# Optimization experiments

Measured on AMD Instinct MI355X. Metric: run time of the kernel, lower is better.

Reference implementation:

```python
import jax, jax.numpy as jnp
import numpy as np

D_MODEL = 512
N_HEADS = 8
HEAD_DIM = D_MODEL // N_HEADS
D_FF = 2048
EPS = 1e-5


def layer_norm(x, gamma, beta):
    mu = jnp.mean(x, axis=-1, keepdims=True)
    var = jnp.mean((x - mu) ** 2, axis=-1, keepdims=True)
    return (x - mu) * jax.lax.rsqrt(var + EPS) * gamma + beta


def setup_inputs() -> dict:
    key = jax.random.key(0)
    ks = jax.random.split(key, 17)
    B, S = 2, 2048
    s_in = 1.0 / np.sqrt(D_MODEL)
    s_ff = 1.0 / np.sqrt(D_FF)
    return {
        "x": jax.random.normal(ks[0], (B, S, D_MODEL), jnp.float32),
        "Wq": jax.random.normal(ks[1], (D_MODEL, D_MODEL), jnp.float32) * s_in,
        "bq": jnp.zeros((D_MODEL,), jnp.float32),
        "Wk": jax.random.normal(ks[2], (D_MODEL, D_MODEL), jnp.float32) * s_in,
        "bk": jnp.zeros((D_MODEL,), jnp.float32),
        "Wv": jax.random.normal(ks[3], (D_MODEL, D_MODEL), jnp.float32) * s_in,
        "bv": jnp.zeros((D_MODEL,), jnp.float32),
        "Wo": jax.random.normal(ks[4], (D_MODEL, D_MODEL), jnp.float32) * s_in,
        "bo": jnp.zeros((D_MODEL,), jnp.float32),
        "W1": jax.random.normal(ks[5], (D_MODEL, D_FF), jnp.float32) * s_in,
        "b1": jnp.zeros((D_FF,), jnp.float32),
        "W2": jax.random.normal(ks[6], (D_FF, D_MODEL), jnp.float32) * s_ff,
        "b2": jnp.zeros((D_MODEL,), jnp.float32),
        "g1": jnp.ones((D_MODEL,), jnp.float32),
        "be1": jnp.zeros((D_MODEL,), jnp.float32),
        "g2": jnp.ones((D_MODEL,), jnp.float32),
        "be2": jnp.zeros((D_MODEL,), jnp.float32),
    }


def reference(x, Wq, bq, Wk, bk, Wv, bv, Wo, bo, W1, b1, W2, b2, g1, be1, g2, be2):
    B, S, _ = x.shape
    # projections + split heads -> [B, H, S, Dh]
    def heads(t):
        return t.reshape(B, S, N_HEADS, HEAD_DIM).transpose(0, 2, 1, 3)
    q = heads(x @ Wq + bq)
    k = heads(x @ Wk + bk)
    v = heads(x @ Wv + bv)
    # explicit scaled dot-product attention (full [B,H,S,S] scores as in source)
    scores = jnp.einsum('bhqd,bhkd->bhqk', q, k) / np.sqrt(HEAD_DIM).astype(np.float32)
    attn = jax.nn.softmax(scores, axis=-1)
    ctx = jnp.einsum('bhqk,bhkd->bhqd', attn, v)
    ctx = ctx.transpose(0, 2, 1, 3).reshape(B, S, D_MODEL)
    attn_out = ctx @ Wo + bo
    # post-norm residual 1
    h = layer_norm(x + attn_out, g1, be1)
    # FFN
    ff = jax.nn.relu(h @ W1 + b1) @ W2 + b2
    # post-norm residual 2
    return layer_norm(h + ff, g2, be2)
```

## Files before the change

kernel.cpp:

```cpp
#include <hip/hip_runtime.h>
#include <cmath>

#define D_MODEL 512
#define N_HEADS 8
#define HEAD_DIM 64
#define D_FF 2048
#define SEQ 2048
#define BATCH 2
#define MROWS (BATCH * SEQ)

typedef __attribute__((ext_vector_type(8))) short short8;
typedef __attribute__((ext_vector_type(4))) float float4v;
typedef unsigned short ushort_t;

static __device__ __forceinline__ ushort_t f2bf(float f) {
    union { float f; unsigned u; } v; v.f = f;
    unsigned r = (v.u + 0x7FFFu + ((v.u >> 16) & 1u)) >> 16;
    return (ushort_t)r;
}
static __device__ __forceinline__ ushort_t f2bf_trunc(float f) {
    union { float f; unsigned u; } v; v.f = f;
    return (ushort_t)(v.u >> 16);
}

static __device__ __forceinline__ void gload16(const void* g, void* l) {
    __builtin_amdgcn_global_load_lds(
        (__attribute__((address_space(1))) void*)(unsigned long long)g,
        (__attribute__((address_space(3))) void*)(unsigned)(unsigned long long)l,
        16, 0, 0);
}

__global__ __launch_bounds__(256) void prep_k(
    const float* __restrict__ x,
    const float* __restrict__ Wq, const float* __restrict__ Wk,
    const float* __restrict__ Wv, const float* __restrict__ Wo,
    const float* __restrict__ W1, const float* __restrict__ W2,
    ushort_t* __restrict__ xb,
    ushort_t* __restrict__ WqkvT, ushort_t* __restrict__ WoT,
    ushort_t* __restrict__ W1T, ushort_t* __restrict__ W2T)
{
    int tile = blockIdx.x;
    if (tile >= 3072) {
        int i = (tile - 3072) * 256 + threadIdx.x;
        float4 f = ((const float4*)x)[i];
        ushort4 o;
        o.x = f2bf(f.x); o.y = f2bf(f.y); o.z = f2bf(f.z); o.w = f2bf(f.w);
        ((ushort4*)xb)[i] = o;
        return;
    }
    const float* src; ushort_t* dst; int Kd, Nd, tloc;
    if (tile < 1024) {
        int wsel = tile >> 8; tloc = tile & 255; Kd = 512; Nd = 512;
        if (wsel == 0)      { src = Wq; dst = WqkvT; }
        else if (wsel == 1) { src = Wk; dst = WqkvT + (size_t)512 * 512; }
        else if (wsel == 2) { src = Wv; dst = WqkvT + (size_t)1024 * 512; }
        else                { src = Wo; dst = WoT; }
    } else if (tile < 2048) { tloc = tile - 1024; Kd = 512;  Nd = 2048; src = W1; dst = W1T; }
    else                    { tloc = tile - 2048; Kd = 2048; Nd = 512;  src = W2; dst = W2T; }
    int tn = Nd >> 5;
    int k0 = (tloc / tn) << 5, n0 = (tloc % tn) << 5;
    __shared__ float tl[32][33];
    int c = threadIdx.x & 31, r = threadIdx.x >> 5;
    #pragma unroll
    for (int i = 0; i < 4; ++i)
        tl[r + i * 8][c] = src[(size_t)(k0 + r + i * 8) * Nd + n0 + c];
    __syncthreads();
    #pragma unroll
    for (int i = 0; i < 4; ++i)
        dst[(size_t)(n0 + r + i * 8) * Kd + k0 + c] = f2bf(tl[c][r + i * 8]);
}

template <int BN, int NT, int MODE>
__global__ __launch_bounds__(256) void gemm_std_k(
    const ushort_t* __restrict__ A, const ushort_t* __restrict__ BT,
    const float* __restrict__ bias, void* __restrict__ Cv,
    int N, int K, int Klen, size_t zstride)
{
    __shared__ ushort_t As[128 * 32];
    __shared__ ushort_t Bs[BN * 32];

    const int t = threadIdx.x;
    const int w = t >> 6, lane = t & 63, l16 = lane & 15, quad = lane >> 4;
    const int m0 = blockIdx.y * 128;
    const int n0 = blockIdx.x * BN;
    const int kbase = blockIdx.z * Klen;
    const int mbase = (w >> 1) * 64;
    const int nbase = (w & 1) * (NT * 16);
    const int srow = lane >> 2;
    const int schk = (lane & 3) * 8;

    float4v acc[4][NT];
    #pragma unroll
    for (int mt = 0; mt < 4; ++mt)
        #pragma unroll
        for (int nt = 0; nt < NT; ++nt)
            acc[mt][nt] = (float4v){0.f, 0.f, 0.f, 0.f};

    for (int ks = kbase; ks < kbase + Klen; ks += 32) {
        __syncthreads();
        #pragma unroll
        for (int g = 0; g < 2; ++g)
            gload16(A + (size_t)(m0 + g * 64 + w * 16 + srow) * K + ks + schk,
                    &As[g * 2048 + w * 512]);
        #pragma unroll
        for (int g = 0; g < BN / 64; ++g)
            gload16(BT + (size_t)(n0 + g * 64 + w * 16 + srow) * K + ks + schk,
                    &Bs[g * 2048 + w * 512]);
        __syncthreads();

        short8 af[4], bf8[NT];
        #pragma unroll
        for (int mt = 0; mt < 4; ++mt)
            af[mt] = *(const short8*)&As[(mbase + mt * 16 + l16) * 32 + quad * 8];
        #pragma unroll
        for (int nt = 0; nt < NT; ++nt)
            bf8[nt] = *(const short8*)&Bs[(nbase + nt * 16 + l16) * 32 + quad * 8];
        #pragma unroll
        for (int mt = 0; mt < 4; ++mt)
            #pragma unroll
            for (int nt = 0; nt < NT; ++nt)
                acc[mt][nt] = __builtin_amdgcn_mfma_f32_16x16x32_bf16(
                    af[mt], bf8[nt], acc[mt][nt], 0, 0, 0);
    }

    float* Cf = (float*)Cv + blockIdx.z * zstride;
    #pragma unroll
    for (int mt = 0; mt < 4; ++mt) {
        #pragma unroll
        for (int nt = 0; nt < NT; ++nt) {
            int gcol = n0 + nbase + nt * 16 + l16;
            float b = (MODE == 2) ? 0.f : bias[gcol];
            #pragma unroll
            for (int r = 0; r < 4; ++r) {
                int grow = m0 + mbase + mt * 16 + quad * 4 + r;
                float v = acc[mt][nt][r] + b;
                if (MODE == 1) v = fmaxf(v, 0.f);
                if (MODE == 1) ((ushort_t*)Cv)[(size_t)grow * N + gcol] = f2bf(v);
                else           Cf[(size_t)grow * N + gcol] = v;
            }
        }
    }
}

__global__ __launch_bounds__(256) void gemm_qkv_k(
    const ushort_t* __restrict__ A, const ushort_t* __restrict__ BT,
    const float* __restrict__ bq, const float* __restrict__ bk,
    const float* __restrict__ bv,
    ushort_t* __restrict__ Qb, ushort_t* __restrict__ Kb,
    ushort_t* __restrict__ VTb)
{
    __shared__ ushort_t As[128 * 32];
    __shared__ ushort_t Bs[128 * 32];

    const int t = threadIdx.x;
    const int w = t >> 6, lane = t & 63, l16 = lane & 15, quad = lane >> 4;
    const int m0 = blockIdx.y * 128;
    const int n0 = blockIdx.x * 128;
    const int mbase = (w >> 1) * 64;
    const int nbase = (w & 1) * 64;
    const int srow = lane >> 2;
    const int schk = (lane & 3) * 8;
    const int K = 512;

    float4v acc[4][4];
    #pragma unroll
    for (int mt = 0; mt < 4; ++mt)
        #pragma unroll
        for (int nt = 0; nt < 4; ++nt)
            acc[mt][nt] = (float4v){0.f, 0.f, 0.f, 0.f};

    for (int ks = 0; ks < 512; ks += 32) {
        __syncthreads();
        #pragma unroll
        for (int g = 0; g < 2; ++g)
            gload16(A + (size_t)(m0 + g * 64 + w * 16 + srow) * K + ks + schk,
                    &As[g * 2048 + w * 512]);
        #pragma unroll
        for (int g = 0; g < 2; ++g)
            gload16(BT + (size_t)(n0 + g * 64 + w * 16 + srow) * K + ks + schk,
                    &Bs[g * 2048 + w * 512]);
        __syncthreads();

        short8 af[4], bf8[4];
        #pragma unroll
        for (int mt = 0; mt < 4; ++mt)
            af[mt] = *(const short8*)&As[(mbase + mt * 16 + l16) * 32 + quad * 8];
        #pragma unroll
        for (int nt = 0; nt < 4; ++nt)
            bf8[nt] = *(const short8*)&Bs[(nbase + nt * 16 + l16) * 32 + quad * 8];
        #pragma unroll
        for (int mt = 0; mt < 4; ++mt)
            #pragma unroll
            for (int nt = 0; nt < 4; ++nt)
                acc[mt][nt] = __builtin_amdgcn_mfma_f32_16x16x32_bf16(
                    af[mt], bf8[nt], acc[mt][nt], 0, 0, 0);
    }

    const int tsel = n0 >> 9;
    const float* bias = (tsel == 0) ? bq : (tsel == 1) ? bk : bv;
    const float scl = (tsel == 0) ? 0.18033688f : 1.0f;
    ushort_t* dst = (tsel == 0) ? Qb : Kb;

    #pragma unroll
    for (int mt = 0; mt < 4; ++mt) {
        #pragma unroll
        for (int nt = 0; nt < 4; ++nt) {
            int gcol = n0 + nbase + nt * 16 + l16;
            int lcol = gcol - (tsel << 9);
            int h = lcol >> 6, dh = lcol & 63;
            float b = bias[lcol];
            #pragma unroll
            for (int r = 0; r < 4; ++r) {
                int grow = m0 + mbase + mt * 16 + quad * 4 + r;
                int bb = grow >> 11, s = grow & 2047;
                float v = (acc[mt][nt][r] + b) * scl;
                if (tsel < 2)
                    dst[(((size_t)(bb * N_HEADS + h)) * SEQ + s) * HEAD_DIM + dh] = f2bf(v);
                else
                    VTb[(((size_t)(bb * N_HEADS + h)) * HEAD_DIM + dh) * SEQ + s] = f2bf(v);
            }
        }
    }
}

__global__ __launch_bounds__(256) void attn_mfma_k(
    const ushort_t* __restrict__ Qg, const ushort_t* __restrict__ Kg,
    const ushort_t* __restrict__ VTg,
    float* __restrict__ Opart, float* __restrict__ Lpart)
{
    __shared__ __align__(16) ushort_t Kbuf[2][64 * 64];
    __shared__ __align__(16) ushort_t Vbuf[2][64 * 64];
    __shared__ __align__(16) ushort_t Ps[4][16 * 64];

    const int bh = blockIdx.x;
    const int q0 = blockIdx.y * 64;
    const int ks = blockIdx.z;
    const int t = threadIdx.x;
    const int w = t >> 6;
    const int lane = t & 63;
    const int l16 = lane & 15;
    const int quad = lane >> 4;
    const int qbase = q0 + w * 16;
    const float M2 = 14.4269504f;

    const int r0 = t >> 3;
    const int r1 = r0 + 32;
    const int g0 = (t & 7) ^ (r0 & 7);
    const int g1 = (t & 7) ^ (r1 & 7);
    const size_t kgrow = (size_t)bh * SEQ;
    const size_t vgrow = (size_t)bh * HEAD_DIM;

#define ATTN_STAGE(b, kb)                                                       \
    {                                                                           \
        gload16(Kg + (kgrow + (kb) + r0) * HEAD_DIM + g0 * 8, &Kbuf[b][w * 512]);          \
        gload16(Kg + (kgrow + (kb) + r1) * HEAD_DIM + g1 * 8, &Kbuf[b][2048 + w * 512]);   \
        gload16(VTg + (vgrow + r0) * SEQ + (kb) + g0 * 8, &Vbuf[b][w * 512]);              \
        gload16(VTg + (vgrow + r1) * SEQ + (kb) + g1 * 8, &Vbuf[b][2048 + w * 512]);       \
    }

    short8 aq[2];
    {
        const ushort_t* qp = Qg + ((size_t)bh * SEQ + qbase + l16) * HEAD_DIM + quad * 8;
        aq[0] = *(const short8*)(qp);
        aq[1] = *(const short8*)(qp + 32);
    }

    float4v o[4] = {};
    float l_acc[4] = {0.f, 0.f, 0.f, 0.f};

    ATTN_STAGE(0, ks * 1024)

    for (int kt = 0; kt < 16; ++kt) {
        const int cur = kt & 1;
        if (kt < 15) {
            ATTN_STAGE(cur ^ 1, ks * 1024 + (kt + 1) * 64)
            asm volatile("s_waitcnt vmcnt(4)" ::: "memory");
        } else {
            asm volatile("s_waitcnt vmcnt(0)" ::: "memory");
        }
        asm volatile("s_barrier" ::: "memory");

        const ushort_t* Kc = Kbuf[cur];
        const ushort_t* Vc = Vbuf[cur];

        float4v s[4];
        #pragma unroll
        for (int nt = 0; nt < 4; ++nt) s[nt] = (float4v){0.f, 0.f, 0.f, 0.f};
        #pragma unroll
        for (int c = 0; c < 2; ++c) {
            const int poff = (((c * 4 + quad) ^ (l16 & 7)) << 3);
            #pragma unroll
            for (int nt = 0; nt < 4; ++nt) {
                short8 bk8 = *(const short8*)&Kc[(nt * 16 + l16) * 64 + poff];
                s[nt] = __builtin_amdgcn_mfma_f32_16x16x32_bf16(aq[c], bk8, s[nt], 0, 0, 0);
            }
        }

        #pragma unroll
        for (int nt = 0; nt < 4; ++nt) {
            #pragma unroll
            for (int r = 0; r < 4; ++r) {
                float p = exp2f(s[nt][r] - M2);
                s[nt][r] = p;
                l_acc[r] += p;
            }
        }

        #pragma unroll
        for (int nt = 0; nt < 4; ++nt)
            #pragma unroll
            for (int r = 0; r < 4; ++r) {
                int row = quad * 4 + r;
                int key = nt * 16 + l16;
                Ps[w][row * 64 + (((key >> 3) ^ (row & 7)) << 3) + (key & 7)] =
                    f2bf_trunc(s[nt][r]);
            }
        asm volatile("s_waitcnt lgkmcnt(0)" ::: "memory");

        #pragma unroll
        for (int c = 0; c < 2; ++c) {
            short8 ap = *(const short8*)&Ps[w][l16 * 64 + ((((c << 2) + quad) ^ (l16 & 7)) << 3)];
            const int poff = (((c * 4 + quad) ^ (l16 & 7)) << 3);
            #pragma unroll
            for (int dt = 0; dt < 4; ++dt) {
                short8 bv8 = *(const short8*)&Vc[(dt * 16 + l16) * 64 + poff];
                o[dt] = __builtin_amdgcn_mfma_f32_16x16x32_bf16(ap, bv8, o[dt], 0, 0, 0);
            }
        }

        asm volatile("s_barrier" ::: "memory");
    }
#undef ATTN_STAGE

    const size_t pbase = ((size_t)(ks * 16 + bh)) * SEQ;
    #pragma unroll
    for (int r = 0; r < 4; ++r) {
        float L = l_acc[r];
        #pragma unroll
        for (int msk = 1; msk < 16; msk <<= 1) L += __shfl_xor(L, msk);
        int qrow = qbase + quad * 4 + r;
        if (l16 == 0) Lpart[pbase + qrow] = L;
        #pragma unroll
        for (int dt = 0; dt < 4; ++dt)
            Opart[(pbase + qrow) * HEAD_DIM + dt * 16 + l16] = o[dt][r];
    }
}

__global__ __launch_bounds__(256) void attn_comb_k(
    const float* __restrict__ Op, const float* __restrict__ Lp,
    ushort_t* __restrict__ ctx)
{
    int g = blockIdx.x * 256 + threadIdx.x;
    int d4 = g & 15;
    int q  = (g >> 4) & 2047;
    int bh = g >> 15;
    float ax = 0.f, ay = 0.f, az = 0.f, aw = 0.f, L = 0.f;
    #pragma unroll
    for (int ks = 0; ks < 2; ++ks) {
        size_t row = ((size_t)(ks * 16 + bh) * SEQ + q) * HEAD_DIM;
        float4 a = ((const float4*)(Op + row))[d4];
        ax += a.x; ay += a.y; az += a.z; aw += a.w;
        L += Lp[ks * 16 * SEQ + bh * SEQ + q];
    }
    float inv = 1.0f / L;
    ushort4 o4;
    o4.x = f2bf(ax * inv);
    o4.y = f2bf(ay * inv);
    o4.z = f2bf(az * inv);
    o4.w = f2bf(aw * inv);
    int bb = bh >> 3, hh = bh & 7;
    *(ushort4*)&ctx[((size_t)(bb * SEQ + q)) * D_MODEL + hh * HEAD_DIM + d4 * 4] = o4;
}

template <int WRITE_BF>
__global__ __launch_bounds__(256) void add_ln_k(
    const float* __restrict__ X, const float* __restrict__ P0,
    const float* __restrict__ P1, const float* __restrict__ bias,
    const float* __restrict__ gam, const float* __restrict__ bet,
    float* __restrict__ O, ushort_t* __restrict__ Ob)
{
    const int row = blockIdx.x;
    const int t = threadIdx.x;
    const size_t ro = (size_t)row * D_MODEL;

    float v0 = X[ro + t]       + P0[ro + t]       + P1[ro + t]       + bias[t];
    float v1 = X[ro + t + 256] + P0[ro + t + 256] + P1[ro + t + 256] + bias[t + 256];
    float s = v0 + v1;
    float ss = v0 * v0 + v1 * v1;
    #pragma unroll
    for (int off = 32; off > 0; off >>= 1) {
        s  += __shfl_down(s, off);
        ss += __shfl_down(ss, off);
    }
    __shared__ float sb[4], ssb[4];
    if ((t & 63) == 0) { sb[t >> 6] = s; ssb[t >> 6] = ss; }
    __syncthreads();
    float S  = sb[0] + sb[1] + sb[2] + sb[3];
    float SS = ssb[0] + ssb[1] + ssb[2] + ssb[3];
    float mu  = S * (1.0f / D_MODEL);
    float var = SS * (1.0f / D_MODEL) - mu * mu;
    float inv = rsqrtf(var + 1e-5f);
    float o0 = (v0 - mu) * inv * gam[t] + bet[t];
    float o1 = (v1 - mu) * inv * gam[t + 256] + bet[t + 256];
    O[ro + t]       = o0;
    O[ro + t + 256] = o1;
    if (WRITE_BF) {
        Ob[ro + t]       = f2bf(o0);
        Ob[ro + t + 256] = f2bf(o1);
    }
}

extern "C" void kernel_launch(void* const* d_in, const int* in_sizes, int n_in,
                              void* d_out, int out_size, void* d_ws, size_t ws_size,
                              hipStream_t stream)
{
    const float* x   = (const float*)d_in[0];
    const float* Wq  = (const float*)d_in[1];
    const float* bq  = (const float*)d_in[2];
    const float* Wk  = (const float*)d_in[3];
    const float* bk  = (const float*)d_in[4];
    const float* Wv  = (const float*)d_in[5];
    const float* bv  = (const float*)d_in[6];
    const float* Wo  = (const float*)d_in[7];
    const float* bo  = (const float*)d_in[8];
    const float* W1  = (const float*)d_in[9];
    const float* b1  = (const float*)d_in[10];
    const float* W2  = (const float*)d_in[11];
    const float* b2  = (const float*)d_in[12];
    const float* g1  = (const float*)d_in[13];
    const float* be1 = (const float*)d_in[14];
    const float* g2  = (const float*)d_in[15];
    const float* be2 = (const float*)d_in[16];
    float* out = (float*)d_out;
    float* ws  = (float*)d_ws;

    ushort_t* WoT   = (ushort_t*)(ws);
    ushort_t* W1T   = (ushort_t*)(ws + 131072);
    ushort_t* W2T   = (ushort_t*)(ws + 655360);
    ushort_t* WqkvT = (ushort_t*)(ws + 1179648);
    ushort_t* xb    = (ushort_t*)(ws + 1572864);
    ushort_t* Qb    = (ushort_t*)(ws + 2621440);
    ushort_t* Kb    = (ushort_t*)(ws + 3670016);
    ushort_t* VTb   = (ushort_t*)(ws + 4718592);
    ushort_t* Ctx   = (ushort_t*)(ws + 5767168);
    float*    Lpart = ws + 6815744;
    float*    Hh    = ws + 6881280;
    float*    P0    = ws + 8978432;
    float*    P1    = ws + 11075584;
    float*    Opart = ws + 8978432;
    ushort_t* FF1   = (ushort_t*)(ws + 1572864);
    ushort_t* Hhb   = (ushort_t*)(ws + 5767168);

    prep_k<<<5120, 256, 0, stream>>>(x, Wq, Wk, Wv, Wo, W1, W2, xb, WqkvT, WoT, W1T, W2T);

    gemm_qkv_k<<<dim3(12, 32), 256, 0, stream>>>(xb, WqkvT, bq, bk, bv, Qb, Kb, VTb);

    attn_mfma_k<<<dim3(16, 32, 2), 256, 0, stream>>>(Qb, Kb, VTb, Opart, Lpart);
    attn_comb_k<<<2048, 256, 0, stream>>>(Opart, Lpart, Ctx);

    gemm_std_k<64, 2, 2><<<dim3(8, 32, 2), 256, 0, stream>>>(
        Ctx, WoT, nullptr, P0, 512, 512, 256, (size_t)MROWS * D_MODEL);

    add_ln_k<1><<<4096, 256, 0, stream>>>(x, P0, P1, bo, g1, be1, Hh, Hhb);

    gemm_std_k<128, 4, 1><<<dim3(16, 32), 256, 0, stream>>>(
        Hhb, W1T, b1, FF1, 2048, 512, 512, 0);

    gemm_std_k<64, 2, 2><<<dim3(8, 32, 2), 256, 0, stream>>>(
        FF1, W2T, nullptr, P0, 512, 2048, 1024, (size_t)MROWS * D_MODEL);

    add_ln_k<0><<<4096, 256, 0, stream>>>(Hh, P0, P1, b2, g2, be2, out, (ushort_t*)nullptr);
}
```

Measured before the change: 229.1 us.

## Fuse the whole layer into one persistent cooperative kernel with grid syncs

```diff
diff --git a/kernel.cpp b/kernel.cpp
--- a/kernel.cpp
+++ b/kernel.cpp
@@ -1,5 +1,8 @@
 #include <hip/hip_runtime.h>
+#include <hip/hip_cooperative_groups.h>
 #include <cmath>
+
+namespace cg = cooperative_groups;
 
 #define D_MODEL 512
 #define N_HEADS 8
@@ -29,6 +32,437 @@
         (__attribute__((address_space(3))) void*)(unsigned)(unsigned long long)l,
         16, 0, 0);
 }
+
+
+template <int MODE>
+__device__ void gemm64_stage(
+    const ushort_t* __restrict__ A, const ushort_t* __restrict__ BT,
+    const float* __restrict__ bias, void* __restrict__ Cv,
+    int N, int K, int m0, int n0, int kbase, int Klen, size_t zoff,
+    ushort_t* __restrict__ sm)
+{
+    ushort_t* As = sm;
+    ushort_t* Bs = sm + 4096;
+
+    const int t = threadIdx.x;
+    const int w = t >> 6, lane = t & 63, l16 = lane & 15, quad = lane >> 4;
+    const int mbase = (w >> 1) * 64;
+    const int nbase = (w & 1) * 32;
+    const int srow = lane >> 2;
+    const int schk = (lane & 3) * 8;
+
+    float4v acc[4][2];
+    #pragma unroll
+    for (int mt = 0; mt < 4; ++mt)
+        #pragma unroll
+        for (int nt = 0; nt < 2; ++nt)
+            acc[mt][nt] = (float4v){0.f, 0.f, 0.f, 0.f};
+
+    for (int ks = kbase; ks < kbase + Klen; ks += 32) {
+        __syncthreads();
+        #pragma unroll
+        for (int g = 0; g < 2; ++g)
+            gload16(A + (size_t)(m0 + g * 64 + w * 16 + srow) * K + ks + schk,
+                    &As[g * 2048 + w * 512]);
+        gload16(BT + (size_t)(n0 + w * 16 + srow) * K + ks + schk, &Bs[w * 512]);
+        __syncthreads();
+
+        short8 af[4], bf8[2];
+        #pragma unroll
+        for (int mt = 0; mt < 4; ++mt)
+            af[mt] = *(const short8*)&As[(mbase + mt * 16 + l16) * 32 + quad * 8];
+        #pragma unroll
+        for (int nt = 0; nt < 2; ++nt)
+            bf8[nt] = *(const short8*)&Bs[(nbase + nt * 16 + l16) * 32 + quad * 8];
+        #pragma unroll
+        for (int mt = 0; mt < 4; ++mt)
+            #pragma unroll
+            for (int nt = 0; nt < 2; ++nt)
+                acc[mt][nt] = __builtin_amdgcn_mfma_f32_16x16x32_bf16(
+                    af[mt], bf8[nt], acc[mt][nt], 0, 0, 0);
+    }
+
+    #pragma unroll
+    for (int mt = 0; mt < 4; ++mt) {
+        #pragma unroll
+        for (int nt = 0; nt < 2; ++nt) {
+            int gcol = n0 + nbase + nt * 16 + l16;
+            float b = (MODE == 2) ? 0.f : bias[gcol];
+            #pragma unroll
+            for (int r = 0; r < 4; ++r) {
+                int grow = m0 + mbase + mt * 16 + quad * 4 + r;
+                float v = acc[mt][nt][r] + b;
+                if (MODE == 1) {
+                    v = fmaxf(v, 0.f);
+                    ((ushort_t*)Cv)[(size_t)grow * N + gcol] = f2bf(v);
+                } else {
+                    ((float*)Cv + zoff)[(size_t)grow * N + gcol] = v;
+                }
+            }
+        }
+    }
+}
+
+__device__ void qkv64_stage(
+    const ushort_t* __restrict__ A, const ushort_t* __restrict__ BT,
+    const float* __restrict__ bq, const float* __restrict__ bk,
+    const float* __restrict__ bv,
+    ushort_t* __restrict__ Qb, ushort_t* __restrict__ Kb,
+    ushort_t* __restrict__ VTb,
+    int m0, int n0, ushort_t* __restrict__ sm)
+{
+    ushort_t* As = sm;
+    ushort_t* Bs = sm + 4096;
+
+    const int t = threadIdx.x;
+    const int w = t >> 6, lane = t & 63, l16 = lane & 15, quad = lane >> 4;
+    const int mbase = (w >> 1) * 64;
+    const int nbase = (w & 1) * 32;
+    const int srow = lane >> 2;
+    const int schk = (lane & 3) * 8;
+    const int K = 512;
+
+    float4v acc[4][2];
+    #pragma unroll
+    for (int mt = 0; mt < 4; ++mt)
+        #pragma unroll
+        for (int nt = 0; nt < 2; ++nt)
+            acc[mt][nt] = (float4v){0.f, 0.f, 0.f, 0.f};
+
+    for (int ks = 0; ks < 512; ks += 32) {
+        __syncthreads();
+        #pragma unroll
+        for (int g = 0; g < 2; ++g)
+            gload16(A + (size_t)(m0 + g * 64 + w * 16 + srow) * K + ks + schk,
+                    &As[g * 2048 + w * 512]);
+        gload16(BT + (size_t)(n0 + w * 16 + srow) * K + ks + schk, &Bs[w * 512]);
+        __syncthreads();
+
+        short8 af[4], bf8[2];
+        #pragma unroll
+        for (int mt = 0; mt < 4; ++mt)
+            af[mt] = *(const short8*)&As[(mbase + mt * 16 + l16) * 32 + quad * 8];
+        #pragma unroll
+        for (int nt = 0; nt < 2; ++nt)
+            bf8[nt] = *(const short8*)&Bs[(nbase + nt * 16 + l16) * 32 + quad * 8];
+        #pragma unroll
+        for (int mt = 0; mt < 4; ++mt)
+            #pragma unroll
+            for (int nt = 0; nt < 2; ++nt)
+                acc[mt][nt] = __builtin_amdgcn_mfma_f32_16x16x32_bf16(
+                    af[mt], bf8[nt], acc[mt][nt], 0, 0, 0);
+    }
+
+    const int tsel = n0 >> 9;
+    const float* bias = (tsel == 0) ? bq : (tsel == 1) ? bk : bv;
+    const float scl = (tsel == 0) ? 0.18033688f : 1.0f;
+    ushort_t* dst = (tsel == 0) ? Qb : Kb;
+
+    #pragma unroll
+    for (int mt = 0; mt < 4; ++mt) {
+        #pragma unroll
+        for (int nt = 0; nt < 2; ++nt) {
+            int gcol = n0 + nbase + nt * 16 + l16;
+            int lcol = gcol - (tsel << 9);
+            int h = lcol >> 6, dh = lcol & 63;
+            float b = bias[lcol];
+            #pragma unroll
+            for (int r = 0; r < 4; ++r) {
+                int grow = m0 + mbase + mt * 16 + quad * 4 + r;
+                int bb = grow >> 11, s = grow & 2047;
+                float v = (acc[mt][nt][r] + b) * scl;
+                if (tsel < 2)
+                    dst[(((size_t)(bb * N_HEADS + h)) * SEQ + s) * HEAD_DIM + dh] = f2bf(v);
+                else
+                    VTb[(((size_t)(bb * N_HEADS + h)) * HEAD_DIM + dh) * SEQ + s] = f2bf(v);
+            }
+        }
+    }
+}
+
+__device__ void attn_stage(
+    const ushort_t* __restrict__ Qg, const ushort_t* __restrict__ Kg,
+    const ushort_t* __restrict__ VTg,
+    float* __restrict__ Opart, float* __restrict__ Lpart,
+    int bh, int q0, int ks, ushort_t* __restrict__ sm)
+{
+    ushort_t* Kbp[2] = { sm, sm + 4096 };
+    ushort_t* Vbp[2] = { sm + 8192, sm + 12288 };
+    const int t = threadIdx.x;
+    const int w = t >> 6;
+    ushort_t* Psw = sm + 16384 + w * 1024;
+
+    const int lane = t & 63;
+    const int l16 = lane & 15;
+    const int quad = lane >> 4;
+    const int qbase = q0 + w * 16;
+    const float M2 = 14.4269504f;
+
+    const int r0 = t >> 3;
+    const int r1 = r0 + 32;
+    const int g0 = (t & 7) ^ (r0 & 7);
+    const int g1 = (t & 7) ^ (r1 & 7);
+    const size_t kgrow = (size_t)bh * SEQ;
+    const size_t vgrow = (size_t)bh * HEAD_DIM;
+
+#define ATTN_ST(b, kb)                                                                     \
+    {                                                                                      \
+        gload16(Kg + (kgrow + (kb) + r0) * HEAD_DIM + g0 * 8, Kbp[b] + w * 512);           \
+        gload16(Kg + (kgrow + (kb) + r1) * HEAD_DIM + g1 * 8, Kbp[b] + 2048 + w * 512);    \
+        gload16(VTg + (vgrow + r0) * SEQ + (kb) + g0 * 8, Vbp[b] + w * 512);               \
+        gload16(VTg + (vgrow + r1) * SEQ + (kb) + g1 * 8, Vbp[b] + 2048 + w * 512);        \
+    }
+
+    short8 aq[2];
+    {
+        const ushort_t* qp = Qg + ((size_t)bh * SEQ + qbase + l16) * HEAD_DIM + quad * 8;
+        aq[0] = *(const short8*)(qp);
+        aq[1] = *(const short8*)(qp + 32);
+    }
+
+    float4v o[4] = {};
+    float l_acc[4] = {0.f, 0.f, 0.f, 0.f};
+
+    ATTN_ST(0, ks * 1024)
+
+    for (int kt = 0; kt < 16; ++kt) {
+        const int cur = kt & 1;
+        if (kt < 15) {
+            ATTN_ST(cur ^ 1, ks * 1024 + (kt + 1) * 64)
+            asm volatile("s_waitcnt vmcnt(4)" ::: "memory");
+        } else {
+            asm volatile("s_waitcnt vmcnt(0)" ::: "memory");
+        }
+        asm volatile("s_barrier" ::: "memory");
+
+        const ushort_t* Kc = Kbp[cur];
+        const ushort_t* Vc = Vbp[cur];
+
+        float4v s[4];
+        #pragma unroll
+        for (int nt = 0; nt < 4; ++nt) s[nt] = (float4v){0.f, 0.f, 0.f, 0.f};
+        #pragma unroll
+        for (int c = 0; c < 2; ++c) {
+            const int poff = (((c * 4 + quad) ^ (l16 & 7)) << 3);
+            #pragma unroll
+            for (int nt = 0; nt < 4; ++nt) {
+                short8 bk8 = *(const short8*)&Kc[(nt * 16 + l16) * 64 + poff];
+                s[nt] = __builtin_amdgcn_mfma_f32_16x16x32_bf16(aq[c], bk8, s[nt], 0, 0, 0);
+            }
+        }
+
+        #pragma unroll
+        for (int nt = 0; nt < 4; ++nt) {
+            #pragma unroll
+            for (int r = 0; r < 4; ++r) {
+                float p = exp2f(s[nt][r] - M2);
+                s[nt][r] = p;
+                l_acc[r] += p;
+            }
+        }
+
+        #pragma unroll
+        for (int nt = 0; nt < 4; ++nt)
+            #pragma unroll
+            for (int r = 0; r < 4; ++r) {
+                int row = quad * 4 + r;
+                int key = nt * 16 + l16;
+                Psw[row * 64 + (((key >> 3) ^ (row & 7)) << 3) + (key & 7)] =
+                    f2bf_trunc(s[nt][r]);
+            }
+        asm volatile("s_waitcnt lgkmcnt(0)" ::: "memory");
+
+        #pragma unroll
+        for (int c = 0; c < 2; ++c) {
+            short8 ap = *(const short8*)&Psw[l16 * 64 + ((((c << 2) + quad) ^ (l16 & 7)) << 3)];
+            const int poff = (((c * 4 + quad) ^ (l16 & 7)) << 3);
+            #pragma unroll
+            for (int dt = 0; dt < 4; ++dt) {
+                short8 bv8 = *(const short8*)&Vc[(dt * 16 + l16) * 64 + poff];
+                o[dt] = __builtin_amdgcn_mfma_f32_16x16x32_bf16(ap, bv8, o[dt], 0, 0, 0);
+            }
+        }
+
+        asm volatile("s_barrier" ::: "memory");
+    }
+#undef ATTN_ST
+
+    const size_t pbase = ((size_t)(ks * 16 + bh)) * SEQ;
+    #pragma unroll
+    for (int r = 0; r < 4; ++r) {
+        float L = l_acc[r];
+        #pragma unroll
+        for (int msk = 1; msk < 16; msk <<= 1) L += __shfl_xor(L, msk);
+        int qrow = qbase + quad * 4 + r;
+        if (l16 == 0) Lpart[pbase + qrow] = L;
+        #pragma unroll
+        for (int dt = 0; dt < 4; ++dt)
+            Opart[(pbase + qrow) * HEAD_DIM + dt * 16 + l16] = o[dt][r];
+    }
+}
+
+template <int WRITE_BF>
+__device__ void ln_stage(
+    const float* __restrict__ X, const float* __restrict__ P0,
+    const float* __restrict__ P1, const float* __restrict__ bias,
+    const float* __restrict__ gam, const float* __restrict__ bet,
+    float* __restrict__ O, ushort_t* __restrict__ Ob, ushort_t* __restrict__ sm)
+{
+    float* sb = (float*)sm;
+    float* ssb = sb + 4;
+    const int t = threadIdx.x;
+    for (int row = blockIdx.x; row < MROWS; row += gridDim.x) {
+        const size_t ro = (size_t)row * D_MODEL;
+        float v0 = X[ro + t]       + P0[ro + t]       + P1[ro + t]       + bias[t];
+        float v1 = X[ro + t + 256] + P0[ro + t + 256] + P1[ro + t + 256] + bias[t + 256];
+        float s = v0 + v1;
+        float ss = v0 * v0 + v1 * v1;
+        #pragma unroll
+        for (int off = 32; off > 0; off >>= 1) {
+            s  += __shfl_down(s, off);
+            ss += __shfl_down(ss, off);
+        }
+        if ((t & 63) == 0) { sb[t >> 6] = s; ssb[t >> 6] = ss; }
+        __syncthreads();
+        float S  = sb[0] + sb[1] + sb[2] + sb[3];
+        float SS = ssb[0] + ssb[1] + ssb[2] + ssb[3];
+        float mu  = S * (1.0f / D_MODEL);
+        float var = SS * (1.0f / D_MODEL) - mu * mu;
+        float inv = rsqrtf(var + 1e-5f);
+        float o0 = (v0 - mu) * inv * gam[t] + bet[t];
+        float o1 = (v1 - mu) * inv * gam[t + 256] + bet[t + 256];
+        O[ro + t]       = o0;
+        O[ro + t + 256] = o1;
+        if (WRITE_BF) {
+            Ob[ro + t]       = f2bf(o0);
+            Ob[ro + t + 256] = f2bf(o1);
+        }
+        __syncthreads();
+    }
+}
+
+__global__ __launch_bounds__(256, 4) void mega_k(
+    const float* x,
+    const float* Wq, const float* bq, const float* Wk, const float* bk,
+    const float* Wv, const float* bv, const float* Wo, const float* bo,
+    const float* W1, const float* b1, const float* W2, const float* b2,
+    const float* g1, const float* be1, const float* g2, const float* be2,
+    float* out, float* ws)
+{
+    cg::grid_group grid = cg::this_grid();
+    __shared__ __align__(16) ushort_t sm[20480];
+
+    ushort_t* WoT   = (ushort_t*)(ws);
+    ushort_t* W1T   = (ushort_t*)(ws + 131072);
+    ushort_t* W2T   = (ushort_t*)(ws + 655360);
+    ushort_t* WqkvT = (ushort_t*)(ws + 1179648);
+    ushort_t* xb    = (ushort_t*)(ws + 1572864);
+    ushort_t* Qb    = (ushort_t*)(ws + 2621440);
+    ushort_t* Kb    = (ushort_t*)(ws + 3670016);
+    ushort_t* VTb   = (ushort_t*)(ws + 4718592);
+    ushort_t* Ctx   = (ushort_t*)(ws + 5767168);
+    float*    Lpart = ws + 6815744;
+    float*    Hh    = ws + 6881280;
+    float*    P0    = ws + 8978432;
+    float*    P1    = ws + 11075584;
+    float*    Opart = ws + 8978432;
+    ushort_t* FF1   = (ushort_t*)(ws + 1572864);
+    ushort_t* Hhb   = (ushort_t*)(ws + 5767168);
+
+    const int bid = blockIdx.x;
+    const int G = gridDim.x;
+    const int t = threadIdx.x;
+
+    for (int tile = bid; tile < 5120; tile += G) {
+        if (tile >= 3072) {
+            int i = (tile - 3072) * 256 + t;
+            float4 f = ((const float4*)x)[i];
+            ushort4 o;
+            o.x = f2bf(f.x); o.y = f2bf(f.y); o.z = f2bf(f.z); o.w = f2bf(f.w);
+            ((ushort4*)xb)[i] = o;
+        } else {
+            const float* src; ushort_t* dst; int Kd, Nd, tloc;
+            if (tile < 1024) {
+                int wsel = tile >> 8; tloc = tile & 255; Kd = 512; Nd = 512;
+                if (wsel == 0)      { src = Wq; dst = WqkvT; }
+                else if (wsel == 1) { src = Wk; dst = WqkvT + (size_t)512 * 512; }
+                else if (wsel == 2) { src = Wv; dst = WqkvT + (size_t)1024 * 512; }
+                else                { src = Wo; dst = WoT; }
+            } else if (tile < 2048) { tloc = tile - 1024; Kd = 512;  Nd = 2048; src = W1; dst = W1T; }
+            else                    { tloc = tile - 2048; Kd = 2048; Nd = 512;  src = W2; dst = W2T; }
+            int tn = Nd >> 5;
+            int k0 = (tloc / tn) << 5, n0 = (tloc % tn) << 5;
+            float* tl = (float*)sm;
+            int c = t & 31, r = t >> 5;
+            #pragma unroll
+            for (int i = 0; i < 4; ++i)
+                tl[(r + i * 8) * 33 + c] = src[(size_t)(k0 + r + i * 8) * Nd + n0 + c];
+            __syncthreads();
+            #pragma unroll
+            for (int i = 0; i < 4; ++i)
+                dst[(size_t)(n0 + r + i * 8) * Kd + k0 + c] = f2bf(tl[c * 33 + r + i * 8]);
+            __syncthreads();
+        }
+    }
+    grid.sync();
+
+    for (int u = bid; u < 768; u += G)
+        qkv64_stage(xb, WqkvT, bq, bk, bv, Qb, Kb, VTb, (u / 24) * 128, (u % 24) * 64, sm);
+    grid.sync();
+
+    for (int u = bid; u < 1024; u += G)
+        attn_stage(Qb, Kb, VTb, Opart, Lpart, u & 15, ((u >> 4) & 31) * 64, u >> 9, sm);
+    grid.sync();
+
+    for (int u = bid; u < 2048; u += G) {
+        int gidx = u * 256 + t;
+        int d4 = gidx & 15;
+        int q  = (gidx >> 4) & 2047;
+        int bh = gidx >> 15;
+        float ax = 0.f, ay = 0.f, az = 0.f, aw = 0.f, L = 0.f;
+        #pragma unroll
+        for (int ks = 0; ks < 2; ++ks) {
+            size_t row = ((size_t)(ks * 16 + bh) * SEQ + q) * HEAD_DIM;
+            float4 a = ((const float4*)(Opart + row))[d4];
+            ax += a.x; ay += a.y; az += a.z; aw += a.w;
+            L += Lpart[ks * 16 * SEQ + bh * SEQ + q];
+        }
+        float inv = 1.0f / L;
+        ushort4 o4;
+        o4.x = f2bf(ax * inv);
+        o4.y = f2bf(ay * inv);
+        o4.z = f2bf(az * inv);
+        o4.w = f2bf(aw * inv);
+        int bb = bh >> 3, hh = bh & 7;
+        *(ushort4*)&Ctx[((size_t)(bb * SEQ + q)) * D_MODEL + hh * HEAD_DIM + d4 * 4] = o4;
+    }
+    grid.sync();
+
+    for (int u = bid; u < 512; u += G) {
+        int n0 = (u & 7) * 64, m0 = ((u >> 3) & 31) * 128, z = u >> 8;
+        gemm64_stage<2>(Ctx, WoT, nullptr, P0, 512, 512, m0, n0, z * 256, 256,
+                        (size_t)z * 2097152, sm);
+    }
+    grid.sync();
+
+    ln_stage<1>(x, P0, P1, bo, g1, be1, Hh, Hhb, sm);
+    grid.sync();
+
+    for (int u = bid; u < 1024; u += G)
+        gemm64_stage<1>(Hhb, W1T, b1, FF1, 2048, 512, (u >> 5) * 128, (u & 31) * 64,
+                        0, 512, 0, sm);
+    grid.sync();
+
+    for (int u = bid; u < 512; u += G) {
+        int n0 = (u & 7) * 64, m0 = ((u >> 3) & 31) * 128, z = u >> 8;
+        gemm64_stage<2>(FF1, W2T, nullptr, P0, 512, 2048, m0, n0, z * 1024, 1024,
+                        (size_t)z * 2097152, sm);
+    }
+    grid.sync();
+
+    ln_stage<0>(Hh, P0, P1, b2, g2, be2, out, (ushort_t*)nullptr, sm);
+}
+
 
 __global__ __launch_bounds__(256) void prep_k(
     const float* __restrict__ x,
@@ -228,122 +662,9 @@
     const ushort_t* __restrict__ VTg,
     float* __restrict__ Opart, float* __restrict__ Lpart)
 {
-    __shared__ __align__(16) ushort_t Kbuf[2][64 * 64];
-    __shared__ __align__(16) ushort_t Vbuf[2][64 * 64];
-    __shared__ __align__(16) ushort_t Ps[4][16 * 64];
-
-    const int bh = blockIdx.x;
-    const int q0 = blockIdx.y * 64;
-    const int ks = blockIdx.z;
-    const int t = threadIdx.x;
-    const int w = t >> 6;
-    const int lane = t & 63;
-    const int l16 = lane & 15;
-    const int quad = lane >> 4;
-    const int qbase = q0 + w * 16;
-    const float M2 = 14.4269504f;
-
-    const int r0 = t >> 3;
-    const int r1 = r0 + 32;
-    const int g0 = (t & 7) ^ (r0 & 7);
-    const int g1 = (t & 7) ^ (r1 & 7);
-    const size_t kgrow = (size_t)bh * SEQ;
-    const size_t vgrow = (size_t)bh * HEAD_DIM;
-
-#define ATTN_STAGE(b, kb)                                                       \
-    {                                                                           \
-        gload16(Kg + (kgrow + (kb) + r0) * HEAD_DIM + g0 * 8, &Kbuf[b][w * 512]);          \
-        gload16(Kg + (kgrow + (kb) + r1) * HEAD_DIM + g1 * 8, &Kbuf[b][2048 + w * 512]);   \
-        gload16(VTg + (vgrow + r0) * SEQ + (kb) + g0 * 8, &Vbuf[b][w * 512]);              \
-        gload16(VTg + (vgrow + r1) * SEQ + (kb) + g1 * 8, &Vbuf[b][2048 + w * 512]);       \
-    }
-
-    short8 aq[2];
-    {
-        const ushort_t* qp = Qg + ((size_t)bh * SEQ + qbase + l16) * HEAD_DIM + quad * 8;
-        aq[0] = *(const short8*)(qp);
-        aq[1] = *(const short8*)(qp + 32);
-    }
-
-    float4v o[4] = {};
-    float l_acc[4] = {0.f, 0.f, 0.f, 0.f};
-
-    ATTN_STAGE(0, ks * 1024)
-
-    for (int kt = 0; kt < 16; ++kt) {
-        const int cur = kt & 1;
-        if (kt < 15) {
-            ATTN_STAGE(cur ^ 1, ks * 1024 + (kt + 1) * 64)
-            asm volatile("s_waitcnt vmcnt(4)" ::: "memory");
-        } else {
-            asm volatile("s_waitcnt vmcnt(0)" ::: "memory");
-        }
-        asm volatile("s_barrier" ::: "memory");
-
-        const ushort_t* Kc = Kbuf[cur];
-        const ushort_t* Vc = Vbuf[cur];
-
-        float4v s[4];
-        #pragma unroll
-        for (int nt = 0; nt < 4; ++nt) s[nt] = (float4v){0.f, 0.f, 0.f, 0.f};
-        #pragma unroll
-        for (int c = 0; c < 2; ++c) {
-            const int poff = (((c * 4 + quad) ^ (l16 & 7)) << 3);
-            #pragma unroll
-            for (int nt = 0; nt < 4; ++nt) {
-                short8 bk8 = *(const short8*)&Kc[(nt * 16 + l16) * 64 + poff];
-                s[nt] = __builtin_amdgcn_mfma_f32_16x16x32_bf16(aq[c], bk8, s[nt], 0, 0, 0);
-            }
-        }
-
-        #pragma unroll
-        for (int nt = 0; nt < 4; ++nt) {
-            #pragma unroll
-            for (int r = 0; r < 4; ++r) {
-                float p = exp2f(s[nt][r] - M2);
-                s[nt][r] = p;
-                l_acc[r] += p;
-            }
-        }
-
-        #pragma unroll
-        for (int nt = 0; nt < 4; ++nt)
-            #pragma unroll
-            for (int r = 0; r < 4; ++r) {
-                int row = quad * 4 + r;
-                int key = nt * 16 + l16;
-                Ps[w][row * 64 + (((key >> 3) ^ (row & 7)) << 3) + (key & 7)] =
-                    f2bf_trunc(s[nt][r]);
-            }
-        asm volatile("s_waitcnt lgkmcnt(0)" ::: "memory");
-
-        #pragma unroll
-        for (int c = 0; c < 2; ++c) {
-            short8 ap = *(const short8*)&Ps[w][l16 * 64 + ((((c << 2) + quad) ^ (l16 & 7)) << 3)];
-            const int poff = (((c * 4 + quad) ^ (l16 & 7)) << 3);
-            #pragma unroll
-            for (int dt = 0; dt < 4; ++dt) {
-                short8 bv8 = *(const short8*)&Vc[(dt * 16 + l16) * 64 + poff];
-                o[dt] = __builtin_amdgcn_mfma_f32_16x16x32_bf16(ap, bv8, o[dt], 0, 0, 0);
-            }
-        }
-
-        asm volatile("s_barrier" ::: "memory");
-    }
-#undef ATTN_STAGE
-
-    const size_t pbase = ((size_t)(ks * 16 + bh)) * SEQ;
-    #pragma unroll
-    for (int r = 0; r < 4; ++r) {
-        float L = l_acc[r];
-        #pragma unroll
-        for (int msk = 1; msk < 16; msk <<= 1) L += __shfl_xor(L, msk);
-        int qrow = qbase + quad * 4 + r;
-        if (l16 == 0) Lpart[pbase + qrow] = L;
-        #pragma unroll
-        for (int dt = 0; dt < 4; ++dt)
-            Opart[(pbase + qrow) * HEAD_DIM + dt * 16 + l16] = o[dt][r];
-    }
+    __shared__ __align__(16) ushort_t smem[20480];
+    attn_stage(Qg, Kg, VTg, Opart, Lpart,
+               blockIdx.x, blockIdx.y * 64, blockIdx.z, smem);
 }
 
 __global__ __launch_bounds__(256) void attn_comb_k(
@@ -434,14 +755,35 @@
     float* out = (float*)d_out;
     float* ws  = (float*)d_ws;
 
+    bool done = false;
+    int dev = 0, coopAttr = 0, occ = 0;
+    (void)hipGetDevice(&dev);
+    (void)hipDeviceGetAttribute(&coopAttr, hipDeviceAttributeCooperativeLaunch, dev);
+    hipError_t eo = hipOccupancyMaxActiveBlocksPerMultiprocessor(&occ, mega_k, 256, 0);
+    if (coopAttr && eo == hipSuccess && occ >= 3) {
+        int G = (occ >= 4) ? 1024 : 768;
+        void* args[] = {
+            (void*)&x,
+            (void*)&Wq, (void*)&bq, (void*)&Wk, (void*)&bk,
+            (void*)&Wv, (void*)&bv, (void*)&Wo, (void*)&bo,
+            (void*)&W1, (void*)&b1, (void*)&W2, (void*)&b2,
+            (void*)&g1, (void*)&be1, (void*)&g2, (void*)&be2,
+            (void*)&out, (void*)&ws
+        };
+        if (hipLaunchCooperativeKernel((const void*)mega_k, dim3(G), dim3(256),
+                                       args, 0, stream) == hipSuccess)
+            done = true;
+    }
+    if (done) return;
+
     ushort_t* WoT   = (ushort_t*)(ws);
     ushort_t* W1T   = (ushort_t*)(ws + 131072);
     ushort_t* W2T   = (ushort_t*)(ws + 655360);
     ushort_t* WqkvT = (ushort_t*)(ws + 1179648);
     ushort_t* xb    = (ushort_t*)(ws + 1572864);
     ushort_t* Qb    = (ushort_t*)(ws + 2621440);
+    ushort_t* VTb   = (ushort_t*)(ws + 4718592);
     ushort_t* Kb    = (ushort_t*)(ws + 3670016);
-    ushort_t* VTb   = (ushort_t*)(ws + 4718592);
     ushort_t* Ctx   = (ushort_t*)(ws + 5767168);
     float*    Lpart = ws + 6815744;
     float*    Hh    = ws + 6881280;
@@ -452,22 +794,15 @@
     ushort_t* Hhb   = (ushort_t*)(ws + 5767168);
 
     prep_k<<<5120, 256, 0, stream>>>(x, Wq, Wk, Wv, Wo, W1, W2, xb, WqkvT, WoT, W1T, W2T);
-
     gemm_qkv_k<<<dim3(12, 32), 256, 0, stream>>>(xb, WqkvT, bq, bk, bv, Qb, Kb, VTb);
-
     attn_mfma_k<<<dim3(16, 32, 2), 256, 0, stream>>>(Qb, Kb, VTb, Opart, Lpart);
     attn_comb_k<<<2048, 256, 0, stream>>>(Opart, Lpart, Ctx);
-
     gemm_std_k<64, 2, 2><<<dim3(8, 32, 2), 256, 0, stream>>>(
         Ctx, WoT, nullptr, P0, 512, 512, 256, (size_t)MROWS * D_MODEL);
-
     add_ln_k<1><<<4096, 256, 0, stream>>>(x, P0, P1, bo, g1, be1, Hh, Hhb);
-
     gemm_std_k<128, 4, 1><<<dim3(16, 32), 256, 0, stream>>>(
         Hhb, W1T, b1, FF1, 2048, 512, 512, 0);
-
     gemm_std_k<64, 2, 2><<<dim3(8, 32, 2), 256, 0, stream>>>(
         FF1, W2T, nullptr, P0, 512, 2048, 1024, (size_t)MROWS * D_MODEL);
-
     add_ln_k<0><<<4096, 256, 0, stream>>>(Hh, P0, P1, b2, g2, be2, out, (ushort_t*)nullptr);
 }
```

New measurement: 246.0 us. +7.4%, slower.
